# Optimization experiments

Hardware: AMD Instinct MI355X
Metric: run time of the kernel (lower is better)

The kernel has to match this reference:

```python
import jax, jax.numpy as jnp
import numpy as np

THETA = 10000.0
R_TOK = 4  # region_token_num


def _local_positions(regions, max_n):
    # 0-based position of each token within its region (count of prior tokens
    # with the same region id) -- order-based, works for any region layout.
    onehot = jax.nn.one_hot(regions, max_n + 1, dtype=jnp.int32)  # [B,T,N+1]
    counts = jnp.cumsum(onehot, axis=1)                            # inclusive
    return jnp.take_along_axis(counts, regions[..., None], axis=-1)[..., 0] - 1


def _rope(q, k, pos, theta):
    # full-head-dim rotary embedding, split-half convention
    D = q.shape[-1]
    inv_freq = 1.0 / (theta ** (jnp.arange(0, D, 2, dtype=jnp.float32) / D))  # [D/2]
    ang = pos[..., None].astype(jnp.float32) * inv_freq                        # [B,S,D/2]
    cos = jnp.tile(jnp.cos(ang), (1, 1, 2))[:, None]                           # [B,1,S,D]
    sin = jnp.tile(jnp.sin(ang), (1, 1, 2))[:, None]

    def rot(x):
        h = x.shape[-1] // 2
        return jnp.concatenate([-x[..., h:], x[..., :h]], axis=-1)

    return q * cos + rot(q) * sin, k * cos + rot(k) * sin


def setup_inputs() -> dict:
    B, H, D = 2, 16, 64
    T, MAX_N = 2048, 64
    P = MAX_N * R_TOK
    key = jax.random.key(0)
    ks = jax.random.split(key, 7)
    f = lambda k, s: jax.random.normal(k, s, dtype=jnp.float32)
    regions = jnp.sort(jax.random.randint(ks[6], (B, T), 1, MAX_N + 1, dtype=jnp.int32), axis=-1)
    return {
        'pool_q': f(ks[0], (B, H, P, D)),
        'pool_k': f(ks[1], (B, H, P, D)),
        'pool_v': f(ks[2], (B, H, P, D)),
        'x_q': f(ks[3], (B, H, T, D)),
        'x_k': f(ks[4], (B, H, T, D)),
        'x_v': f(ks[5], (B, H, T, D)),
        'regions': regions,
        't_mask': jnp.ones((B, T), dtype=bool),
        'n_mask': jnp.ones((B, MAX_N), dtype=bool),
        'max_n': MAX_N,
    }


def reference(pool_q, pool_k, pool_v, x_q, x_k, x_v, regions, t_mask, n_mask, max_n):
    B, H, P, D = pool_q.shape
    R = R_TOK
    # sequence = [pool, x]
    q = jnp.concatenate([pool_q, x_q], axis=2)
    k = jnp.concatenate([pool_k, x_k], axis=2)
    v = jnp.concatenate([pool_v, x_v], axis=2)

    # local-mode positions (use_pool_offset=False -> pool tokens at pos 0)
    pool_pos = jnp.zeros((B, P), dtype=jnp.int32)
    x_pos = (_local_positions(regions, max_n) + R) * (regions > 0).astype(jnp.int32)
    pos = jnp.concatenate([pool_pos, x_pos], axis=-1)  # [B,S]
    q, k = _rope(q, k, pos, THETA)

    # block-local (same-region) mask: [B,1,S,S], True = allowed
    pool_region = jnp.broadcast_to(jnp.repeat(jnp.arange(1, max_n + 1, dtype=jnp.int32), R)[None], (B, P))
    pool_valid = jnp.repeat(n_mask, R, axis=1)                      # [B,P]
    full_region = jnp.concatenate([pool_region, regions], axis=-1)  # [B,S]
    full_valid = jnp.concatenate([pool_valid, t_mask], axis=-1)     # [B,S]
    same = full_region[:, :, None] == full_region[:, None, :]
    valid = full_valid[:, :, None] & full_valid[:, None, :]
    nonpad = (full_region != 0)[:, :, None] & (full_region != 0)[:, None, :]
    mask = (same & valid & nonpad)[:, None]                          # [B,1,S,S]

    scores = jnp.einsum('bhqd,bhkd->bhqk', q, k) / jnp.sqrt(jnp.float32(D))
    scores = jnp.where(mask, scores, jnp.float32(-1e9))
    attn = jax.nn.softmax(scores, axis=-1)
    out = jnp.einsum('bhqk,bhkd->bhqd', attn, v)
    return out[:, :, :P, :]
```

## Files before the change

kernel.cpp:

```cpp
#include <hip/hip_runtime.h>
#include <hip/hip_bf16.h>

#define BB   2
#define HH   16
#define DD   64
#define TT   2048
#define MAXN 64
#define RTOK 4
#define PP   (MAXN * RTOK)
#define VPAD 68

__global__ __launch_bounds__(256)
void build_ranges(const int* __restrict__ regions, int* __restrict__ tab) {
    const int b   = blockIdx.x;
    const int tid = threadIdx.x;
    const int* reg = regions + b * TT;
    int* t = tab + b * 66;
    const int i0 = tid * 8;
    int v[9];
    const int4 a0 = *(const int4*)(reg + i0);
    const int4 a1 = *(const int4*)(reg + i0 + 4);
    v[0] = a0.x; v[1] = a0.y; v[2] = a0.z; v[3] = a0.w;
    v[4] = a1.x; v[5] = a1.y; v[6] = a1.z; v[7] = a1.w;
    v[8] = (tid == 255) ? (MAXN + 1) : reg[i0 + 8];
    if (tid == 0)
        for (int rr = 1; rr <= v[0]; ++rr) t[rr] = 0;
    #pragma unroll
    for (int j = 0; j < 8; ++j)
        for (int rr = v[j] + 1; rr <= v[j + 1]; ++rr) t[rr] = i0 + j + 1;
}

__global__ __launch_bounds__(256, 6)
void lapd_attn(const float* __restrict__ pool_q,
               const float* __restrict__ pool_k,
               const float* __restrict__ pool_v,
               const float* __restrict__ x_k,
               const float* __restrict__ x_v,
               const int* __restrict__ tab,
               float* __restrict__ out) {
    const int blk   = blockIdx.x;
    const int r_idx = blk & (MAXN - 1);
    const int bh    = blk >> 6;
    const int b     = bh / HH;

    const int tid  = threadIdx.x;
    const int wave = tid >> 6;
    const int lane = tid & 63;

    __shared__ float v_t[DD][VPAD];
    __shared__ float q_s[4][DD];
    __shared__ float p_s[4][64];

    const int* tb   = tab + b * 66;
    const int start = tb[r_idx + 1];
    const int cnt   = tb[r_idx + 2] - start;
    const int sstart = (cnt > 0) ? start : 0;

    const size_t poolbase = ((size_t)bh * PP + r_idx * RTOK) * DD;
    const float* pk = pool_k + poolbase;
    const float* pv = pool_v + poolbase;
    const float* xk = x_k + (size_t)bh * TT * DD;
    const float* xv = x_v + (size_t)bh * TT * DD;

    const size_t qidx = poolbase + (size_t)(wave * DD) + lane;
    const float qv = pool_q[qidx] * 0.125f;

    const int key0 = tid >> 4;
    const int d    = (tid & 15) * 4;

    float invf[4];
    #pragma unroll
    for (int c = 0; c < 4; ++c)
        invf[c] = __expf((float)((d + c) & 31) * (-9.210340371976184f / 32.0f));
    const float sgn = (d < 32) ? -1.0f : 1.0f;

    q_s[wave][lane] = qv;
    __syncthreads();

    float qr[4][4];
    #pragma unroll
    for (int w = 0; w < 4; ++w)
        #pragma unroll
        for (int c = 0; c < 4; ++c)
            qr[w][c] = q_s[w][d + c];

    float acc = 0.0f, l = 0.0f;
    int xbase = 0;
    bool first = true;

    for (;;) {
        const int koff = first ? RTOK : 0;
        int nx = cnt - xbase;
        if (nx > 64 - koff) nx = 64 - koff;
        const int tn = koff + (nx > 0 ? nx : 0);

        #pragma unroll
        for (int half = 0; half < 2; ++half) {
            float4 kv[2], vv[2];
            int keyv[2], xiv[2];
            #pragma unroll
            for (int i = 0; i < 2; ++i) {
                const int key = key0 + (half * 2 + i) * 16;
                keyv[i] = key;
                int xi = key - koff;
                if (xi > nx - 1) xi = nx - 1;
                if (xi < 0) xi = 0;
                xiv[i] = xi;
                if (first && key < RTOK) {
                    kv[i] = *(const float4*)(pk + key * DD + d);
                    vv[i] = *(const float4*)(pv + key * DD + d);
                } else {
                    const size_t off = (size_t)(sstart + xbase + xi) * DD;
                    kv[i] = *(const float4*)(xk + off + d);
                    vv[i] = *(const float4*)(xv + off + d);
                }
            }
            #pragma unroll
            for (int i = 0; i < 2; ++i) {
                const int key = keyv[i];
                float4 kp;
                kp.x = __shfl_xor(kv[i].x, 8, 64);
                kp.y = __shfl_xor(kv[i].y, 8, 64);
                kp.z = __shfl_xor(kv[i].z, 8, 64);
                kp.w = __shfl_xor(kv[i].w, 8, 64);
                float kr[4] = {kv[i].x, kv[i].y, kv[i].z, kv[i].w};
                if (!(first && key < RTOK)) {
                    const float pos = (float)(xbase + xiv[i] + RTOK);
                    const float kpd[4] = {kp.x, kp.y, kp.z, kp.w};
                    #pragma unroll
                    for (int c = 0; c < 4; ++c) {
                        float sv, cv;
                        __sincosf(pos * invf[c], &sv, &cv);
                        kr[c] = kr[c] * cv + sgn * kpd[c] * sv;
                    }
                }
                v_t[d + 0][key] = vv[i].x;
                v_t[d + 1][key] = vv[i].y;
                v_t[d + 2][key] = vv[i].z;
                v_t[d + 3][key] = vv[i].w;
                float s0 = qr[0][0]*kr[0] + qr[0][1]*kr[1] + qr[0][2]*kr[2] + qr[0][3]*kr[3];
                float s1 = qr[1][0]*kr[0] + qr[1][1]*kr[1] + qr[1][2]*kr[2] + qr[1][3]*kr[3];
                float s2 = qr[2][0]*kr[0] + qr[2][1]*kr[1] + qr[2][2]*kr[2] + qr[2][3]*kr[3];
                float s3 = qr[3][0]*kr[0] + qr[3][1]*kr[1] + qr[3][2]*kr[2] + qr[3][3]*kr[3];
                #pragma unroll
                for (int off = 1; off <= 8; off <<= 1) {
                    s0 += __shfl_xor(s0, off, 64);
                    s1 += __shfl_xor(s1, off, 64);
                    s2 += __shfl_xor(s2, off, 64);
                    s3 += __shfl_xor(s3, off, 64);
                }
                const int sub = lane & 15;
                if (sub < 4) {
                    const float sq = (sub == 0) ? s0 : (sub == 1) ? s1
                                   : (sub == 2) ? s2 : s3;
                    p_s[sub][key] = (key < tn) ? __expf(sq) : 0.0f;
                }
            }
        }
        __syncthreads();

        float a0 = 0, a1 = 0, a2 = 0, a3 = 0, l0 = 0;
        #pragma unroll
        for (int k = 0; k < 64; k += 4) {
            const float4 v4 = *(const float4*)&v_t[lane][k];
            const float p0 = p_s[wave][k + 0];
            const float p1 = p_s[wave][k + 1];
            const float p2 = p_s[wave][k + 2];
            const float p3 = p_s[wave][k + 3];
            a0 += p0 * v4.x;
            a1 += p1 * v4.y;
            a2 += p2 * v4.z;
            a3 += p3 * v4.w;
            l0 += (p0 + p1) + (p2 + p3);
        }
        acc += (a0 + a1) + (a2 + a3);
        l   += l0;

        xbase += (nx > 0 ? nx : 0);
        first = false;
        if (xbase >= cnt) break;
        __syncthreads();
    }

    out[qidx] = acc / l;
}

extern "C" void kernel_launch(void* const* d_in, const int* in_sizes, int n_in,
                              void* d_out, int out_size, void* d_ws, size_t ws_size,
                              hipStream_t stream) {
    const float* pool_q  = (const float*)d_in[0];
    const float* pool_k  = (const float*)d_in[1];
    const float* pool_v  = (const float*)d_in[2];
    const float* x_k     = (const float*)d_in[4];
    const float* x_v     = (const float*)d_in[5];
    const int*   regions = (const int*)d_in[6];
    float*       out     = (float*)d_out;
    int*         tab     = (int*)d_ws;

    build_ranges<<<dim3(BB), dim3(256), 0, stream>>>(regions, tab);
    lapd_attn<<<dim3(BB * HH * MAXN), dim3(256), 0, stream>>>(
        pool_q, pool_k, pool_v, x_k, x_v, tab, out);
}
```

Before: 124.1 us.

## Stage RoPE-rotated keys in shared memory and compute scores per wave

```diff
diff --git a/kernel.cpp b/kernel.cpp
--- a/kernel.cpp
+++ b/kernel.cpp
@@ -8,7 +8,7 @@
 #define MAXN 64
 #define RTOK 4
 #define PP   (MAXN * RTOK)
-#define VPAD 68
+#define PAD  68
 
 __global__ __launch_bounds__(256)
 void build_ranges(const int* __restrict__ regions, int* __restrict__ tab) {
@@ -30,7 +30,7 @@
         for (int rr = v[j] + 1; rr <= v[j + 1]; ++rr) t[rr] = i0 + j + 1;
 }
 
-__global__ __launch_bounds__(256, 6)
+__global__ __launch_bounds__(256, 4)
 void lapd_attn(const float* __restrict__ pool_q,
                const float* __restrict__ pool_k,
                const float* __restrict__ pool_v,
@@ -47,14 +47,10 @@
     const int wave = tid >> 6;
     const int lane = tid & 63;
 
-    __shared__ float v_t[DD][VPAD];
+    __shared__ float k_s[64][PAD];
+    __shared__ float v_t[DD][PAD];
     __shared__ float q_s[4][DD];
     __shared__ float p_s[4][64];
-
-    const int* tb   = tab + b * 66;
-    const int start = tb[r_idx + 1];
-    const int cnt   = tb[r_idx + 2] - start;
-    const int sstart = (cnt > 0) ? start : 0;
 
     const size_t poolbase = ((size_t)bh * PP + r_idx * RTOK) * DD;
     const float* pk = pool_k + poolbase;
@@ -64,25 +60,20 @@
 
     const size_t qidx = poolbase + (size_t)(wave * DD) + lane;
     const float qv = pool_q[qidx] * 0.125f;
+    q_s[wave][lane] = qv;
 
-    const int key0 = tid >> 4;
-    const int d    = (tid & 15) * 4;
+    const int* tb    = tab + b * 66;
+    const int start  = tb[r_idx + 1];
+    const int cnt    = tb[r_idx + 2] - start;
+    const int sstart = (cnt > 0) ? start : 0;
+
+    const int kA = tid >> 3;
+    const int d  = (tid & 7) * 4;
 
     float invf[4];
     #pragma unroll
     for (int c = 0; c < 4; ++c)
-        invf[c] = __expf((float)((d + c) & 31) * (-9.210340371976184f / 32.0f));
-    const float sgn = (d < 32) ? -1.0f : 1.0f;
-
-    q_s[wave][lane] = qv;
-    __syncthreads();
-
-    float qr[4][4];
-    #pragma unroll
-    for (int w = 0; w < 4; ++w)
-        #pragma unroll
-        for (int c = 0; c < 4; ++c)
-            qr[w][c] = q_s[w][d + c];
+        invf[c] = __expf((float)(d + c) * (-9.210340371976184f / 32.0f));
 
     float acc = 0.0f, l = 0.0f;
     int xbase = 0;
@@ -94,70 +85,63 @@
         if (nx > 64 - koff) nx = 64 - koff;
         const int tn = koff + (nx > 0 ? nx : 0);
 
+        float4 klo[2], khi[2], vlo[2], vhi[2];
+        int xiv[2];
+        bool ispool[2];
         #pragma unroll
-        for (int half = 0; half < 2; ++half) {
-            float4 kv[2], vv[2];
-            int keyv[2], xiv[2];
-            #pragma unroll
-            for (int i = 0; i < 2; ++i) {
-                const int key = key0 + (half * 2 + i) * 16;
-                keyv[i] = key;
-                int xi = key - koff;
-                if (xi > nx - 1) xi = nx - 1;
-                if (xi < 0) xi = 0;
-                xiv[i] = xi;
-                if (first && key < RTOK) {
-                    kv[i] = *(const float4*)(pk + key * DD + d);
-                    vv[i] = *(const float4*)(pv + key * DD + d);
-                } else {
-                    const size_t off = (size_t)(sstart + xbase + xi) * DD;
-                    kv[i] = *(const float4*)(xk + off + d);
-                    vv[i] = *(const float4*)(xv + off + d);
+        for (int i = 0; i < 2; ++i) {
+            const int key = kA + i * 32;
+            int xi = key - koff;
+            if (xi > nx - 1) xi = nx - 1;
+            if (xi < 0) xi = 0;
+            xiv[i] = xi;
+            ispool[i] = first && (key < RTOK);
+            const float* kbase = ispool[i] ? (pk + key * DD)
+                               : (xk + (size_t)(sstart + xbase + xi) * DD);
+            const float* vbase = ispool[i] ? (pv + key * DD)
+                               : (xv + (size_t)(sstart + xbase + xi) * DD);
+            klo[i] = *(const float4*)(kbase + d);
+            khi[i] = *(const float4*)(kbase + d + 32);
+            vlo[i] = *(const float4*)(vbase + d);
+            vhi[i] = *(const float4*)(vbase + d + 32);
+        }
+        #pragma unroll
+        for (int i = 0; i < 2; ++i) {
+            const int key = kA + i * 32;
+            float rlo[4] = {klo[i].x, klo[i].y, klo[i].z, klo[i].w};
+            float rhi[4] = {khi[i].x, khi[i].y, khi[i].z, khi[i].w};
+            if (!ispool[i]) {
+                const float pos = (float)(xbase + xiv[i] + RTOK);
+                #pragma unroll
+                for (int c = 0; c < 4; ++c) {
+                    float sv, cv;
+                    __sincosf(pos * invf[c], &sv, &cv);
+                    const float lo = rlo[c], hi = rhi[c];
+                    rlo[c] = lo * cv - hi * sv;
+                    rhi[c] = hi * cv + lo * sv;
                 }
             }
-            #pragma unroll
-            for (int i = 0; i < 2; ++i) {
-                const int key = keyv[i];
-                float4 kp;
-                kp.x = __shfl_xor(kv[i].x, 8, 64);
-                kp.y = __shfl_xor(kv[i].y, 8, 64);
-                kp.z = __shfl_xor(kv[i].z, 8, 64);
-                kp.w = __shfl_xor(kv[i].w, 8, 64);
-                float kr[4] = {kv[i].x, kv[i].y, kv[i].z, kv[i].w};
-                if (!(first && key < RTOK)) {
-                    const float pos = (float)(xbase + xiv[i] + RTOK);
-                    const float kpd[4] = {kp.x, kp.y, kp.z, kp.w};
-                    #pragma unroll
-                    for (int c = 0; c < 4; ++c) {
-                        float sv, cv;
-                        __sincosf(pos * invf[c], &sv, &cv);
-                        kr[c] = kr[c] * cv + sgn * kpd[c] * sv;
-                    }
-                }
-                v_t[d + 0][key] = vv[i].x;
-                v_t[d + 1][key] = vv[i].y;
-                v_t[d + 2][key] = vv[i].z;
-                v_t[d + 3][key] = vv[i].w;
-                float s0 = qr[0][0]*kr[0] + qr[0][1]*kr[1] + qr[0][2]*kr[2] + qr[0][3]*kr[3];
-                float s1 = qr[1][0]*kr[0] + qr[1][1]*kr[1] + qr[1][2]*kr[2] + qr[1][3]*kr[3];
-                float s2 = qr[2][0]*kr[0] + qr[2][1]*kr[1] + qr[2][2]*kr[2] + qr[2][3]*kr[3];
-                float s3 = qr[3][0]*kr[0] + qr[3][1]*kr[1] + qr[3][2]*kr[2] + qr[3][3]*kr[3];
-                #pragma unroll
-                for (int off = 1; off <= 8; off <<= 1) {
-                    s0 += __shfl_xor(s0, off, 64);
-                    s1 += __shfl_xor(s1, off, 64);
-                    s2 += __shfl_xor(s2, off, 64);
-                    s3 += __shfl_xor(s3, off, 64);
-                }
-                const int sub = lane & 15;
-                if (sub < 4) {
-                    const float sq = (sub == 0) ? s0 : (sub == 1) ? s1
-                                   : (sub == 2) ? s2 : s3;
-                    p_s[sub][key] = (key < tn) ? __expf(sq) : 0.0f;
-                }
-            }
+            *(float4*)&k_s[key][d]      = make_float4(rlo[0], rlo[1], rlo[2], rlo[3]);
+            *(float4*)&k_s[key][d + 32] = make_float4(rhi[0], rhi[1], rhi[2], rhi[3]);
+            v_t[d + 0][key] = vlo[i].x;  v_t[d + 32][key] = vhi[i].x;
+            v_t[d + 1][key] = vlo[i].y;  v_t[d + 33][key] = vhi[i].y;
+            v_t[d + 2][key] = vlo[i].z;  v_t[d + 34][key] = vhi[i].z;
+            v_t[d + 3][key] = vlo[i].w;  v_t[d + 35][key] = vhi[i].w;
         }
         __syncthreads();
+
+        float s0 = 0, s1 = 0, s2 = 0, s3 = 0;
+        #pragma unroll
+        for (int dd2 = 0; dd2 < DD; dd2 += 4) {
+            const float4 kk = *(const float4*)&k_s[lane][dd2];
+            const float4 qq = *(const float4*)&q_s[wave][dd2];
+            s0 += qq.x * kk.x;
+            s1 += qq.y * kk.y;
+            s2 += qq.z * kk.z;
+            s3 += qq.w * kk.w;
+        }
+        const float s = (s0 + s1) + (s2 + s3);
+        p_s[wave][lane] = (lane < tn) ? __expf(s) : 0.0f;
 
         float a0 = 0, a1 = 0, a2 = 0, a3 = 0, l0 = 0;
         #pragma unroll
```

Measured after the change: 115.1 us. 1.08x faster.
